# Performance work log

Measured on AMD Instinct MI355X. Metric: run time of the kernel, lower is better.

## Reference

```python
import jax, jax.numpy as jnp
import numpy as np

B, S, D = 2, 2048, 1024
H = 16
DK = D // H
LW = 256          # local window size
GSTRIDE = 64      # global downsample stride
SW = 512          # sliding window size
EPS = 1e-5
SCALE = 1.0 / np.sqrt(DK)


def _layernorm(x, g, b):
    mu = jnp.mean(x, axis=-1, keepdims=True)
    var = jnp.mean(jnp.square(x - mu), axis=-1, keepdims=True)
    return (x - mu) * jax.lax.rsqrt(var + EPS) * g + b


def setup_inputs() -> dict:
    key = jax.random.key(0)
    ks = jax.random.split(key, 16)
    std = 0.02
    def lin(k, din, dout):
        kw, kb = jax.random.split(k)
        return (jax.random.normal(kw, (din, dout), jnp.float32) * std,
                jax.random.normal(kb, (dout,), jnp.float32) * std)
    inp = {}
    inp["x"] = jax.random.normal(ks[0], (B, S, D), jnp.float32)
    # hierarchical attention params
    inp["lq_w"], inp["lq_b"] = lin(ks[1], D, D)
    inp["lk_w"], inp["lk_b"] = lin(ks[2], D, D)
    inp["lv_w"], inp["lv_b"] = lin(ks[3], D, D)
    inp["gq_w"], inp["gq_b"] = lin(ks[4], D, D)
    inp["gk_w"], inp["gk_b"] = lin(ks[5], D, D)
    inp["gv_w"], inp["gv_b"] = lin(ks[6], D, D)
    inp["h_out_w"], inp["h_out_b"] = lin(ks[7], 2 * D, D)
    inp["h_ln_g"] = jnp.ones((D,), jnp.float32)
    inp["h_ln_b"] = jnp.zeros((D,), jnp.float32)
    # sliding window attention params
    inp["sq_w"], inp["sq_b"] = lin(ks[8], D, D)
    inp["sk_w"], inp["sk_b"] = lin(ks[9], D, D)
    inp["sv_w"], inp["sv_b"] = lin(ks[10], D, D)
    inp["s_out_w"], inp["s_out_b"] = lin(ks[11], D, D)
    # combination
    inp["comb_w"], inp["comb_b"] = lin(ks[12], 2 * D, D)
    inp["ln_g"] = jnp.ones((D,), jnp.float32)
    inp["ln_b"] = jnp.zeros((D,), jnp.float32)
    return inp


def _forward(x, lq_w, lq_b, lk_w, lk_b, lv_w, lv_b,
             gq_w, gq_b, gk_w, gk_b, gv_w, gv_b,
             h_out_w, h_out_b, h_ln_g, h_ln_b,
             sq_w, sq_b, sk_w, sk_b, sv_w, sv_b,
             s_out_w, s_out_b, comb_w, comb_b, ln_g, ln_b):
    nw = S // LW  # seq_len is a multiple of LW (no padding needed)

    # ---- Hierarchical: local windowed attention (vectorized over windows) ----
    xw = x.reshape(B, nw, LW, D)
    lq = (xw @ lq_w + lq_b).reshape(B, nw, LW, H, DK)
    lk = (xw @ lk_w + lk_b).reshape(B, nw, LW, H, DK)
    lv = (xw @ lv_w + lv_b).reshape(B, nw, LW, H, DK)
    lsc = jnp.einsum('bnqhd,bnkhd->bnhqk', lq, lk) * SCALE
    lat = jax.nn.softmax(lsc, axis=-1)
    local_out = jnp.einsum('bnhqk,bnkhd->bnqhd', lat, lv).reshape(B, S, D)

    # ---- Hierarchical: global attention over strided downsample ----
    gc = x[:, ::GSTRIDE]                 # [B, G, D], G = S // GSTRIDE
    G = gc.shape[1]
    gq = (x @ gq_w + gq_b).reshape(B, S, H, DK)
    gk = (gc @ gk_w + gk_b).reshape(B, G, H, DK)
    gv = (gc @ gv_w + gv_b).reshape(B, G, H, DK)
    gsc = jnp.einsum('bqhd,bkhd->bhqk', gq, gk) * SCALE
    gat = jax.nn.softmax(gsc, axis=-1)
    global_out = jnp.einsum('bhqk,bkhd->bqhd', gat, gv).reshape(B, S, D)

    h_comb = jnp.concatenate([local_out, global_out], axis=-1) @ h_out_w + h_out_b
    h_out = _layernorm(x + h_comb, h_ln_g, h_ln_b)

    # ---- Sliding window attention ----
    sq = (x @ sq_w + sq_b).reshape(B, S, H, DK)
    sk = (x @ sk_w + sk_b).reshape(B, S, H, DK)
    sv = (x @ sv_w + sv_b).reshape(B, S, H, DK)
    ssc = jnp.einsum('bqhd,bkhd->bhqk', sq, sk) * SCALE
    idx = jnp.arange(S)
    half = SW // 2
    band = jnp.abs(idx[:, None] - idx[None, :]) <= half   # [S, S]
    ssc = jnp.where(band[None, None], ssc, -jnp.inf)
    sat = jax.nn.softmax(ssc, axis=-1)
    s_attn = jnp.einsum('bhqk,bkhd->bqhd', sat, sv).reshape(B, S, D)
    s_out = s_attn @ s_out_w + s_out_b

    # ---- combine scales ----
    combined = jnp.concatenate([h_out, s_out], axis=-1) @ comb_w + comb_b
    return _layernorm(x + combined, ln_g, ln_b)


def reference(x, lq_w, lq_b, lk_w, lk_b, lv_w, lv_b,
              gq_w, gq_b, gk_w, gk_b, gv_w, gv_b,
              h_out_w, h_out_b, h_ln_g, h_ln_b,
              sq_w, sq_b, sk_w, sk_b, sv_w, sv_b,
              s_out_w, s_out_b, comb_w, comb_b, ln_g, ln_b):
    return _forward(x, lq_w, lq_b, lk_w, lk_b, lv_w, lv_b,
                    gq_w, gq_b, gk_w, gk_b, gv_w, gv_b,
                    h_out_w, h_out_b, h_ln_g, h_ln_b,
                    sq_w, sq_b, sk_w, sk_b, sv_w, sv_b,
                    s_out_w, s_out_b, comb_w, comb_b, ln_g, ln_b)
```

## Files before the change

### kernel.cpp

```cpp
#include <hip/hip_runtime.h>

#define BATCH 2
#define SEQ   2048
#define DIM   1024
#define NH    16
#define DK    64
#define SCALE_F 0.125f
#define MASKED  -2e30f
#define MINIT   -1e30f

typedef __attribute__((ext_vector_type(4))) float f4;
typedef __attribute__((ext_vector_type(4))) float f32x4;
typedef __attribute__((ext_vector_type(8))) short s16x8;
typedef __attribute__((ext_vector_type(4))) int  i32x4;
typedef __attribute__((ext_vector_type(4))) unsigned short u16x4;

__device__ __forceinline__ float bf2f(unsigned short u){ return __uint_as_float(((unsigned)u) << 16); }
__device__ __forceinline__ unsigned short f2bf(float f){
  unsigned u = __float_as_uint(f);
  u += 0x7FFFu + ((u >> 16) & 1u);
  return (unsigned short)(u >> 16);
}

#define ASYNC_LDS16(g, l) \
  __builtin_amdgcn_global_load_lds((const __attribute__((address_space(1))) void*)(g), \
                                   (__attribute__((address_space(3))) void*)(l), 16, 0, 0)

__global__ __launch_bounds__(256) void cast_bf16_kernel(const float* __restrict__ in,
                                                        unsigned short* __restrict__ out, int n){
  int i = (blockIdx.x * 256 + threadIdx.x) * 4;
  if (i < n){
    f4 v = *(const f4*)&in[i];
    u16x4 o = { f2bf(v[0]), f2bf(v[1]), f2bf(v[2]), f2bf(v[3]) };
    *(u16x4*)&out[i] = o;
  }
}

struct TCP { const float* w[12]; unsigned short* wt[12]; };
__global__ __launch_bounds__(256) void transpose_cast_b(TCP P, int K){
  const float* W = P.w[blockIdx.z];
  unsigned short* Wt = P.wt[blockIdx.z];
  __shared__ float tile[32][33];
  int x = threadIdx.x & 31, y = threadIdx.x >> 5;
  int bc = blockIdx.x << 5;
  int br = blockIdx.y << 5;
  #pragma unroll
  for (int yy = y; yy < 32; yy += 8)
    tile[yy][x] = W[(size_t)(br + yy) * DIM + bc + x];
  __syncthreads();
  #pragma unroll
  for (int yy = y; yy < 32; yy += 8)
    Wt[(size_t)(bc + yy) * K + br + x] = f2bf(tile[x][yy]);
}

__global__ __launch_bounds__(256) void gc_extract(const float* __restrict__ x,
                                                  unsigned short* __restrict__ gcb){
  int row = blockIdx.x;
  int t = threadIdx.x;
  unsigned short* dst = gcb + (size_t)row * DIM;
  if (row < BATCH * 32){
    int b = row >> 5, g = row & 31;
    const float* src = x + ((size_t)b * SEQ + (size_t)g * 64) * DIM;
    f4 v = *(const f4*)&src[t * 4];
    u16x4 o = { f2bf(v[0]), f2bf(v[1]), f2bf(v[2]), f2bf(v[3]) };
    *(u16x4*)&dst[t * 4] = o;
  } else {
    u16x4 z = { 0, 0, 0, 0 };
    *(u16x4*)&dst[t * 4] = z;
  }
}

struct GOut { unsigned short* ob; float* of; const float* bias; int ld; int tr; };
struct GOuts { GOut d[4]; };

template<int BN>
__global__ __launch_bounds__(256) void gemm_bf16(
    const unsigned short* __restrict__ A, const unsigned short* __restrict__ Bt,
    GOuts descs, int K)
{
  constexpr int NF = BN / 32;
  __shared__ __align__(16) unsigned short As[2][128 * 32];
  __shared__ __align__(16) unsigned short Bs[2][BN * 32];
  const int tid = threadIdx.x;
  const int lane = tid & 63;
  const int w = tid >> 6;
  const int wr = w >> 1, wc = w & 1;
  const int gx = gridDim.x;
  const int nwg = gx * gridDim.y;
  const int orig = blockIdx.y * gx + blockIdx.x;
  const int swz = (orig & 7) * (nwg >> 3) + (orig >> 3);
  const int tx = swz % gx, ty = swz / gx;
  const int tm = ty << 7, tn = tx * BN;
  const GOut dsc = descs.d[tn >> 10];
  const int trans = dsc.tr;

  const int r0 = tid >> 2;
  const int ksw = (((tid & 3) ^ ((tid >> 3) & 3)) << 3);
  const unsigned short* Ag0 = A + (size_t)(tm + r0) * K + ksw;
  const unsigned short* Ag1 = A + (size_t)(tm + r0 + 64) * K + ksw;
  const unsigned short* Bg0 = Bt + (size_t)(tn + r0) * K + ksw;
  const unsigned short* Bg1 = Bt + (size_t)(tn + r0 + 64) * K + ksw;

  f32x4 acc[4][NF];
  #pragma unroll
  for (int m = 0; m < 4; ++m)
    #pragma unroll
    for (int n = 0; n < NF; ++n) acc[m][n] = (f32x4){0.f, 0.f, 0.f, 0.f};

  const int fr = lane & 15, fg = lane >> 4;
  const int kro = ((fg ^ ((fr >> 1) & 3)) << 3);

  auto STAGE = [&](int buf, int t){
    const int kk = t * 32;
    ASYNC_LDS16(Ag0 + kk, &As[buf][w * 512]);
    ASYNC_LDS16(Ag1 + kk, &As[buf][w * 512 + 2048]);
    ASYNC_LDS16(Bg0 + kk, &Bs[buf][w * 512]);
    if constexpr (BN == 128) ASYNC_LDS16(Bg1 + kk, &Bs[buf][w * 512 + 2048]);
  };
  auto COMPUTE = [&](int buf){
    s16x8 af[4], bfv[NF];
    #pragma unroll
    for (int m = 0; m < 4; ++m)
      af[m] = *(const s16x8*)&As[buf][(wr * 64 + m * 16 + fr) * 32 + kro];
    #pragma unroll
    for (int n = 0; n < NF; ++n)
      bfv[n] = *(const s16x8*)&Bs[buf][(wc * (BN / 2) + n * 16 + fr) * 32 + kro];
    if (trans){
      #pragma unroll
      for (int m = 0; m < 4; ++m)
        #pragma unroll
        for (int n = 0; n < NF; ++n)
          acc[m][n] = __builtin_amdgcn_mfma_f32_16x16x32_bf16(bfv[n], af[m], acc[m][n], 0, 0, 0);
    } else {
      #pragma unroll
      for (int m = 0; m < 4; ++m)
        #pragma unroll
        for (int n = 0; n < NF; ++n)
          acc[m][n] = __builtin_amdgcn_mfma_f32_16x16x32_bf16(af[m], bfv[n], acc[m][n], 0, 0, 0);
    }
  };

  const int nt = K >> 5;
  STAGE(0, 0);
  STAGE(1, 1);
  for (int t = 0; t < nt - 1; ++t){
    const int cur = t & 1;
    if constexpr (BN == 128) asm volatile("s_waitcnt vmcnt(4)" ::: "memory");
    else                     asm volatile("s_waitcnt vmcnt(3)" ::: "memory");
    __builtin_amdgcn_s_barrier();
    __builtin_amdgcn_sched_barrier(0);
    COMPUTE(cur);
    __builtin_amdgcn_sched_barrier(0);
    __builtin_amdgcn_s_barrier();
    __builtin_amdgcn_sched_barrier(0);
    if (t + 2 < nt) STAGE(cur, t + 2);
  }
  asm volatile("s_waitcnt vmcnt(0)" ::: "memory");
  __builtin_amdgcn_s_barrier();
  __builtin_amdgcn_sched_barrier(0);
  COMPUTE((nt - 1) & 1);

  #pragma unroll
  for (int m = 0; m < 4; ++m){
    #pragma unroll
    for (int n = 0; n < NF; ++n){
      if (!trans){
        int cl = (tn + wc * (BN / 2) + n * 16 + fr) & 1023;
        float bv = dsc.bias ? dsc.bias[cl] : 0.f;
        #pragma unroll
        for (int r = 0; r < 4; ++r){
          int row = tm + wr * 64 + m * 16 + fg * 4 + r;
          float v = acc[m][n][r] + bv;
          if (dsc.of) dsc.of[(size_t)row * dsc.ld + cl] = v;
          if (dsc.ob) dsc.ob[(size_t)row * dsc.ld + cl] = f2bf(v);
        }
      } else {
        int colT = tm + wr * 64 + m * 16 + fr;
        #pragma unroll
        for (int r = 0; r < 4; ++r){
          int dl = (tn + wc * (BN / 2) + n * 16 + fg * 4 + r) & 1023;
          float v = acc[m][n][r] + (dsc.bias ? dsc.bias[dl] : 0.f);
          dsc.ob[(size_t)dl * dsc.ld + colT] = f2bf(v);
        }
      }
    }
  }
}

template<int MODE>
__global__ __launch_bounds__(256) void mfma_attn(
    const unsigned short* __restrict__ Qb,
    const unsigned short* __restrict__ Kb,
    const unsigned short* __restrict__ Vtb, int ldvt,
    unsigned short* __restrict__ Out, int ldo, int ocol)
{
  __shared__ __align__(16) unsigned short Ks[64][72];
  __shared__ __align__(16) unsigned short Vs[64][72];
  __shared__ __align__(16) unsigned short Pl[4][16][72];
  const int tid = threadIdx.x, lane = tid & 63, wv = tid >> 6;
  const int fr = lane & 15, fg = lane >> 4;
  const int blk = blockIdx.x;
  const int h  = blk & 15;
  const int qc = (blk >> 4) & 31;
  const int b  = blk >> 9;
  const int q0 = qc * 64;
  const int tq0 = b * SEQ + q0;
  int jlo, ntile;
  if (MODE == 0){ jlo = (qc >> 2) << 8; ntile = 4; }
  else if (MODE == 1){
    jlo = q0 - 256 < 0 ? 0 : q0 - 256;
    int jhi = q0 + 320 > SEQ ? SEQ : q0 + 320;
    ntile = (jhi - jlo) >> 6;
  } else { jlo = 0; ntile = 1; }
  const int ktok0 = (MODE == 2) ? b * 32 : b * SEQ;

  s16x8 qf[2];
  {
    const size_t qrow = (size_t)(tq0 + wv * 16 + fr) * DIM + h * DK;
    qf[0] = *(const s16x8*)&Qb[qrow + fg * 8];
    qf[1] = *(const s16x8*)&Qb[qrow + 32 + fg * 8];
  }
  f32x4 of[4];
  #pragma unroll
  for (int dt = 0; dt < 4; ++dt) of[dt] = (f32x4){0.f, 0.f, 0.f, 0.f};
  f32x4 m4 = (f32x4){MINIT, MINIT, MINIT, MINIT};
  f32x4 l4 = (f32x4){0.f, 0.f, 0.f, 0.f};

  for (int t = 0; t < ntile; ++t){
    const int jb = jlo + t * 64;
    __syncthreads();
    #pragma unroll
    for (int p = 0; p < 2; ++p){
      int idx = p * 256 + tid;
      int row = idx >> 3, c8 = idx & 7;
      *(i32x4*)&Ks[row][c8 * 8] =
          *(const i32x4*)&Kb[(size_t)(ktok0 + jb + row) * DIM + h * DK + c8 * 8];
      i32x4 v = *(const i32x4*)&Vtb[(size_t)(h * DK + row) * ldvt + ktok0 + jb + c8 * 8];
      *(i32x4*)((char*)Vs + row * 144 + ((c8 * 16) ^ ((row & 7) << 4))) = v;
    }
    __syncthreads();
    f32x4 sf[4];
    #pragma unroll
    for (int t16 = 0; t16 < 4; ++t16){
      sf[t16] = (f32x4){0.f, 0.f, 0.f, 0.f};
      #pragma unroll
      for (int ks = 0; ks < 2; ++ks){
        s16x8 kf = *(const s16x8*)&Ks[t16 * 16 + fr][ks * 32 + fg * 8];
        sf[t16] = __builtin_amdgcn_mfma_f32_16x16x32_bf16(qf[ks], kf, sf[t16], 0, 0, 0);
      }
    }
    #pragma unroll
    for (int t16 = 0; t16 < 4; ++t16){
      int j = jb + t16 * 16 + fr;
      #pragma unroll
      for (int r = 0; r < 4; ++r){
        float v = sf[t16][r] * SCALE_F;
        bool valid = true;
        if (MODE == 1){ int dq = (q0 + wv * 16 + fg * 4 + r) - j; valid = (dq <= 256) && (dq >= -256); }
        if (MODE == 2){ valid = j < 32; }
        sf[t16][r] = valid ? v : MASKED;
      }
    }
    f32x4 mx;
    #pragma unroll
    for (int r = 0; r < 4; ++r)
      mx[r] = fmaxf(fmaxf(sf[0][r], sf[1][r]), fmaxf(sf[2][r], sf[3][r]));
    #pragma unroll
    for (int off = 1; off < 16; off <<= 1){
      #pragma unroll
      for (int r = 0; r < 4; ++r) mx[r] = fmaxf(mx[r], __shfl_xor(mx[r], off));
    }
    f32x4 sc;
    #pragma unroll
    for (int r = 0; r < 4; ++r){
      float mn = fmaxf(m4[r], mx[r]);
      sc[r] = __expf(m4[r] - mn);
      m4[r] = mn;
    }
    f32x4 sm = (f32x4){0.f, 0.f, 0.f, 0.f};
    #pragma unroll
    for (int t16 = 0; t16 < 4; ++t16){
      #pragma unroll
      for (int r = 0; r < 4; ++r){
        float e = __expf(sf[t16][r] - m4[r]);
        sm[r] += e;
        Pl[wv][fg * 4 + r][t16 * 16 + fr] = f2bf(e);
      }
    }
    #pragma unroll
    for (int off = 1; off < 16; off <<= 1){
      #pragma unroll
      for (int r = 0; r < 4; ++r) sm[r] += __shfl_xor(sm[r], off);
    }
    #pragma unroll
    for (int r = 0; r < 4; ++r) l4[r] = l4[r] * sc[r] + sm[r];
    #pragma unroll
    for (int dt = 0; dt < 4; ++dt)
      #pragma unroll
      for (int r = 0; r < 4; ++r) of[dt][r] *= sc[r];
    #pragma unroll
    for (int ks2 = 0; ks2 < 2; ++ks2){
      s16x8 pa = *(const s16x8*)&Pl[wv][fr][ks2 * 32 + fg * 8];
      #pragma unroll
      for (int dt = 0; dt < 4; ++dt){
        int d = dt * 16 + fr;
        s16x8 vf = *(const s16x8*)((char*)Vs + d * 144 + ((ks2 * 64 + fg * 16) ^ ((d & 7) << 4)));
        of[dt] = __builtin_amdgcn_mfma_f32_16x16x32_bf16(pa, vf, of[dt], 0, 0, 0);
      }
    }
  }
  #pragma unroll
  for (int dt = 0; dt < 4; ++dt){
    #pragma unroll
    for (int r = 0; r < 4; ++r){
      float val = of[dt][r] / l4[r];
      int q = tq0 + wv * 16 + fg * 4 + r;
      Out[(size_t)q * ldo + ocol + h * DK + dt * 16 + fr] = f2bf(val);
    }
  }
}

__global__ __launch_bounds__(256) void ln_fused(
    const float* __restrict__ x, const float* __restrict__ dlt,
    const float* __restrict__ g, const float* __restrict__ bta,
    float* __restrict__ outf, unsigned short* __restrict__ outb, int ldo)
{
  const int row = blockIdx.x;
  const int t = threadIdx.x, lane = t & 63, wv = t >> 6;
  const float* xr = x + (size_t)row * DIM;
  const float* dr = dlt + (size_t)row * DIM;
  f4 xv = *(const f4*)&xr[t * 4];
  f4 dv = *(const f4*)&dr[t * 4];
  f4 y = xv + dv;
  float s = y[0] + y[1] + y[2] + y[3];
  float ss = y[0]*y[0] + y[1]*y[1] + y[2]*y[2] + y[3]*y[3];
  #pragma unroll
  for (int off = 1; off < 64; off <<= 1){ s += __shfl_xor(s, off); ss += __shfl_xor(ss, off); }
  __shared__ float red[8];
  if (lane == 0){ red[wv] = s; red[wv + 4] = ss; }
  __syncthreads();
  float S = red[0] + red[1] + red[2] + red[3];
  float SS = red[4] + red[5] + red[6] + red[7];
  float mu = S * (1.f / DIM);
  float var = SS * (1.f / DIM) - mu * mu;
  float rs = rsqrtf(var + 1e-5f);
  f4 gv = *(const f4*)&g[t * 4];
  f4 bv = *(const f4*)&bta[t * 4];
  f4 o;
  #pragma unroll
  for (int i = 0; i < 4; ++i) o[i] = (y[i] - mu) * rs * gv[i] + bv[i];
  if (outf) *(f4*)&outf[(size_t)row * ldo + t * 4] = o;
  if (outb){
    u16x4 ob = { f2bf(o[0]), f2bf(o[1]), f2bf(o[2]), f2bf(o[3]) };
    *(u16x4*)&outb[(size_t)row * ldo + t * 4] = ob;
  }
}

extern "C" void kernel_launch(void* const* d_in, const int* in_sizes, int n_in,
                              void* d_out, int out_size, void* d_ws, size_t ws_size,
                              hipStream_t stream){
  (void)in_sizes; (void)n_in; (void)out_size; (void)ws_size;
  const float* x      = (const float*)d_in[0];
  const float* lq_w   = (const float*)d_in[1];  const float* lq_b  = (const float*)d_in[2];
  const float* lk_w   = (const float*)d_in[3];  const float* lk_b  = (const float*)d_in[4];
  const float* lv_w   = (const float*)d_in[5];  const float* lv_b  = (const float*)d_in[6];
  const float* gq_w   = (const float*)d_in[7];  const float* gq_b  = (const float*)d_in[8];
  const float* gk_w   = (const float*)d_in[9];  const float* gk_b  = (const float*)d_in[10];
  const float* gv_w   = (const float*)d_in[11]; const float* gv_b  = (const float*)d_in[12];
  const float* ho_w   = (const float*)d_in[13]; const float* ho_b  = (const float*)d_in[14];
  const float* hln_g  = (const float*)d_in[15]; const float* hln_b = (const float*)d_in[16];
  const float* sq_w   = (const float*)d_in[17]; const float* sq_b  = (const float*)d_in[18];
  const float* sk_w   = (const float*)d_in[19]; const float* sk_b  = (const float*)d_in[20];
  const float* sv_w   = (const float*)d_in[21]; const float* sv_b  = (const float*)d_in[22];
  const float* so_w   = (const float*)d_in[23]; const float* so_b  = (const float*)d_in[24];
  const float* cb_w   = (const float*)d_in[25]; const float* cb_b  = (const float*)d_in[26];
  const float* ln_g   = (const float*)d_in[27]; const float* ln_b  = (const float*)d_in[28];

  const size_t M = (size_t)BATCH * SEQ;
  const size_t W1 = (size_t)DIM * DIM;
  char* ws = (char*)d_ws;
  size_t off = 0;
  auto alloc = [&](size_t bytes) -> void* {
    void* p = ws + off; off += (bytes + 255) & ~(size_t)255; return p;
  };
  unsigned short* xb    = (unsigned short*)alloc(M * DIM * 2);
  unsigned short* wt_s  = (unsigned short*)alloc(3 * W1 * 2);
  unsigned short* wt_lg = (unsigned short*)alloc(4 * W1 * 2);
  unsigned short* wt_g2 = (unsigned short*)alloc(2 * W1 * 2);
  unsigned short* wt_so = (unsigned short*)alloc(W1 * 2);
  unsigned short* wt_ho = (unsigned short*)alloc(2 * W1 * 2);
  unsigned short* wt_cb = (unsigned short*)alloc(2 * W1 * 2);
  unsigned short* gcb   = (unsigned short*)alloc((size_t)128 * DIM * 2);
  unsigned short* qb    = (unsigned short*)alloc(M * DIM * 2);
  unsigned short* kb    = (unsigned short*)alloc(M * DIM * 2);
  unsigned short* vtb   = (unsigned short*)alloc(M * DIM * 2);
  unsigned short* qg    = (unsigned short*)alloc(M * DIM * 2);
  unsigned short* gkb   = (unsigned short*)alloc((size_t)128 * DIM * 2);
  unsigned short* vtg   = (unsigned short*)alloc((size_t)128 * DIM * 2);
  unsigned short* satt  = (unsigned short*)alloc(M * DIM * 2);
  unsigned short* hcat  = (unsigned short*)alloc(M * 2 * DIM * 2);
  unsigned short* ccat  = (unsigned short*)alloc(M * 2 * DIM * 2);
  float* Af             = (float*)alloc(M * DIM * 4);

  dim3 b256(256);
  cast_bf16_kernel<<<dim3((M * DIM) / 1024), b256, 0, stream>>>(x, xb, (int)(M * DIM));
  {
    TCP p1 = {};
    const float* ws_[10] = {sq_w, sk_w, sv_w, lq_w, lk_w, lv_w, gq_w, gk_w, gv_w, so_w};
    unsigned short* wts_[10] = {wt_s, wt_s + W1, wt_s + 2 * W1,
                                wt_lg, wt_lg + W1, wt_lg + 2 * W1, wt_lg + 3 * W1,
                                wt_g2, wt_g2 + W1, wt_so};
    for (int i = 0; i < 10; ++i){ p1.w[i] = ws_[i]; p1.wt[i] = wts_[i]; }
    transpose_cast_b<<<dim3(32, 32, 10), b256, 0, stream>>>(p1, DIM);
    TCP p2 = {};
    p2.w[0] = ho_w; p2.wt[0] = wt_ho;
    p2.w[1] = cb_w; p2.wt[1] = wt_cb;
    transpose_cast_b<<<dim3(32, 64, 2), b256, 0, stream>>>(p2, 2 * DIM);
  }
  gc_extract<<<dim3(128), b256, 0, stream>>>(x, gcb);

  dim3 attn_grid(1024);
  auto mk = [&](unsigned short* ob, float* of, const float* bias, int ld, int tr) -> GOut {
    GOut g; g.ob = ob; g.of = of; g.bias = bias; g.ld = ld; g.tr = tr; return g;
  };

  {
    GOuts ds = {};
    ds.d[0] = mk(qb,  nullptr, sq_b, DIM, 0);
    ds.d[1] = mk(kb,  nullptr, sk_b, DIM, 0);
    ds.d[2] = mk(vtb, nullptr, sv_b, (int)M, 1);
    gemm_bf16<128><<<dim3(24, 32), b256, 0, stream>>>(xb, wt_s, ds, DIM);
  }
  mfma_attn<1><<<attn_grid, b256, 0, stream>>>(qb, kb, vtb, (int)M, satt, DIM, 0);

  {
    GOuts ds = {};
    ds.d[0] = mk(qb,  nullptr, lq_b, DIM, 0);
    ds.d[1] = mk(kb,  nullptr, lk_b, DIM, 0);
    ds.d[2] = mk(vtb, nullptr, lv_b, (int)M, 1);
    ds.d[3] = mk(qg,  nullptr, gq_b, DIM, 0);
    gemm_bf16<128><<<dim3(32, 32), b256, 0, stream>>>(xb, wt_lg, ds, DIM);
  }
  {
    GOuts ds = {};
    ds.d[0] = mk(ccat + 1024, nullptr, so_b, 2 * DIM, 0);
    gemm_bf16<64><<<dim3(16, 32), b256, 0, stream>>>(satt, wt_so, ds, DIM);
  }
  mfma_attn<0><<<attn_grid, b256, 0, stream>>>(qb, kb, vtb, (int)M, hcat, 2 * DIM, 0);

  {
    GOuts ds = {};
    ds.d[0] = mk(gkb, nullptr, gk_b, DIM, 0);
    ds.d[1] = mk(vtg, nullptr, gv_b, 128, 1);
    gemm_bf16<128><<<dim3(16, 1), b256, 0, stream>>>(gcb, wt_g2, ds, DIM);
  }
  mfma_attn<2><<<attn_grid, b256, 0, stream>>>(qg, gkb, vtg, 128, hcat, 2 * DIM, 1024);

  {
    GOuts ds = {};
    ds.d[0] = mk(nullptr, Af, ho_b, DIM, 0);
    gemm_bf16<64><<<dim3(16, 32), b256, 0, stream>>>(hcat, wt_ho, ds, 2 * DIM);
  }
  ln_fused<<<dim3((int)M), b256, 0, stream>>>(x, Af, hln_g, hln_b, nullptr, ccat, 2 * DIM);

  {
    GOuts ds = {};
    ds.d[0] = mk(nullptr, Af, cb_b, DIM, 0);
    gemm_bf16<64><<<dim3(16, 32), b256, 0, stream>>>(ccat, wt_cb, ds, 2 * DIM);
  }
  ln_fused<<<dim3((int)M), b256, 0, stream>>>(x, Af, ln_g, ln_b, (float*)d_out, nullptr, DIM);
}
```

Baseline: 525.2 us.

## Add 256x256-tile 512-thread GEMM kernel for fused QKV projections

Adds a new bf16 MFMA GEMM kernel with 256x256 output tiles, 8 waves, double-buffered async LDS staging with an XOR swizzle, and a grouped tile-order remap. It replaces the 128-tile GEMM for the sliding-window QKV projection and the local/global QKV projection. The larger tiles raise arithmetic intensity and cut global reloads of A and B. The cost is fewer workgroups (192 and 256 blocks), which may underfill the CUs, and 128 KB of LDS per block, which is likely to limit occupancy below the requested two blocks per CU.

```diff
diff --git a/kernel.cpp b/kernel.cpp
--- a/kernel.cpp
+++ b/kernel.cpp
@@ -179,6 +179,125 @@
         #pragma unroll
         for (int r = 0; r < 4; ++r){
           int dl = (tn + wc * (BN / 2) + n * 16 + fg * 4 + r) & 1023;
+          float v = acc[m][n][r] + (dsc.bias ? dsc.bias[dl] : 0.f);
+          dsc.ob[(size_t)dl * dsc.ld + colT] = f2bf(v);
+        }
+      }
+    }
+  }
+}
+
+__global__ __launch_bounds__(512, 2) void gemm256(
+    const unsigned short* __restrict__ A, const unsigned short* __restrict__ Bt,
+    GOuts descs, int K)
+{
+  __shared__ __align__(16) unsigned short As[2][256 * 64];
+  __shared__ __align__(16) unsigned short Bs[2][256 * 64];
+  const int tid = threadIdx.x;
+  const int lane = tid & 63;
+  const int w = tid >> 6;
+  const int wr = w >> 2, wc = w & 3;
+  const int gx = gridDim.x;
+  const int nwg = gx * gridDim.y;
+  const int orig = blockIdx.y * gx + blockIdx.x;
+  const int swz = (orig & 7) * (nwg >> 3) + (orig >> 3);
+  const int tx = swz % gx, ty = swz / gx;
+  const int tm = ty << 8, tn = tx << 8;
+  const GOut dsc = descs.d[tn >> 10];
+  const int trans = dsc.tr;
+
+  const int sr = lane >> 3;
+  const int klog = (((lane & 7) ^ sr) << 3);
+  const unsigned short* Agp[4];
+  const unsigned short* Bgp[4];
+  #pragma unroll
+  for (int i = 0; i < 4; ++i){
+    const int s = w * 4 + i;
+    Agp[i] = A + (size_t)(tm + s * 8 + sr) * K + klog;
+    Bgp[i] = Bt + (size_t)(tn + s * 8 + sr) * K + klog;
+  }
+
+  f32x4 acc[8][4];
+  #pragma unroll
+  for (int m = 0; m < 8; ++m)
+    #pragma unroll
+    for (int n = 0; n < 4; ++n) acc[m][n] = (f32x4){0.f, 0.f, 0.f, 0.f};
+
+  const int fr = lane & 15, fg = lane >> 4;
+
+  auto STAGE = [&](int buf, int t){
+    const int kk = t * 64;
+    #pragma unroll
+    for (int i = 0; i < 4; ++i){
+      ASYNC_LDS16(Agp[i] + kk, &As[buf][(w * 4 + i) * 512]);
+      ASYNC_LDS16(Bgp[i] + kk, &Bs[buf][(w * 4 + i) * 512]);
+    }
+  };
+  auto COMPUTE = [&](int buf){
+    #pragma unroll
+    for (int ks = 0; ks < 2; ++ks){
+      const int rc = (((ks * 4 + fg) ^ (fr & 7)) << 3);
+      s16x8 af[8], bfv[4];
+      #pragma unroll
+      for (int m = 0; m < 8; ++m)
+        af[m] = *(const s16x8*)&As[buf][(wr * 128 + m * 16 + fr) * 64 + rc];
+      #pragma unroll
+      for (int n = 0; n < 4; ++n)
+        bfv[n] = *(const s16x8*)&Bs[buf][(wc * 64 + n * 16 + fr) * 64 + rc];
+      if (trans){
+        #pragma unroll
+        for (int m = 0; m < 8; ++m)
+          #pragma unroll
+          for (int n = 0; n < 4; ++n)
+            acc[m][n] = __builtin_amdgcn_mfma_f32_16x16x32_bf16(bfv[n], af[m], acc[m][n], 0, 0, 0);
+      } else {
+        #pragma unroll
+        for (int m = 0; m < 8; ++m)
+          #pragma unroll
+          for (int n = 0; n < 4; ++n)
+            acc[m][n] = __builtin_amdgcn_mfma_f32_16x16x32_bf16(af[m], bfv[n], acc[m][n], 0, 0, 0);
+      }
+    }
+  };
+
+  const int nt = K >> 6;
+  STAGE(0, 0);
+  STAGE(1, 1);
+  for (int t = 0; t < nt - 1; ++t){
+    const int cur = t & 1;
+    asm volatile("s_waitcnt vmcnt(8)" ::: "memory");
+    __builtin_amdgcn_s_barrier();
+    __builtin_amdgcn_sched_barrier(0);
+    COMPUTE(cur);
+    __builtin_amdgcn_sched_barrier(0);
+    __builtin_amdgcn_s_barrier();
+    __builtin_amdgcn_sched_barrier(0);
+    if (t + 2 < nt) STAGE(cur, t + 2);
+  }
+  asm volatile("s_waitcnt vmcnt(0)" ::: "memory");
+  __builtin_amdgcn_s_barrier();
+  __builtin_amdgcn_sched_barrier(0);
+  COMPUTE((nt - 1) & 1);
+
+  #pragma unroll
+  for (int m = 0; m < 8; ++m){
+    #pragma unroll
+    for (int n = 0; n < 4; ++n){
+      if (!trans){
+        int cl = (tn + wc * 64 + n * 16 + fr) & 1023;
+        float bv = dsc.bias ? dsc.bias[cl] : 0.f;
+        #pragma unroll
+        for (int r = 0; r < 4; ++r){
+          int row = tm + wr * 128 + m * 16 + fg * 4 + r;
+          float v = acc[m][n][r] + bv;
+          if (dsc.of) dsc.of[(size_t)row * dsc.ld + cl] = v;
+          if (dsc.ob) dsc.ob[(size_t)row * dsc.ld + cl] = f2bf(v);
+        }
+      } else {
+        int colT = tm + wr * 128 + m * 16 + fr;
+        #pragma unroll
+        for (int r = 0; r < 4; ++r){
+          int dl = (tn + wc * 64 + n * 16 + fg * 4 + r) & 1023;
           float v = acc[m][n][r] + (dsc.bias ? dsc.bias[dl] : 0.f);
           dsc.ob[(size_t)dl * dsc.ld + colT] = f2bf(v);
         }
@@ -403,6 +522,7 @@
   float* Af             = (float*)alloc(M * DIM * 4);
 
   dim3 b256(256);
+  dim3 b512(512);
   cast_bf16_kernel<<<dim3((M * DIM) / 1024), b256, 0, stream>>>(x, xb, (int)(M * DIM));
   {
     TCP p1 = {};
@@ -429,7 +549,7 @@
     ds.d[0] = mk(qb,  nullptr, sq_b, DIM, 0);
     ds.d[1] = mk(kb,  nullptr, sk_b, DIM, 0);
     ds.d[2] = mk(vtb, nullptr, sv_b, (int)M, 1);
-    gemm_bf16<128><<<dim3(24, 32), b256, 0, stream>>>(xb, wt_s, ds, DIM);
+    gemm256<<<dim3(12, 16), b512, 0, stream>>>(xb, wt_s, ds, DIM);
   }
   mfma_attn<1><<<attn_grid, b256, 0, stream>>>(qb, kb, vtb, (int)M, satt, DIM, 0);
 
@@ -439,7 +559,7 @@
     ds.d[1] = mk(kb,  nullptr, lk_b, DIM, 0);
     ds.d[2] = mk(vtb, nullptr, lv_b, (int)M, 1);
     ds.d[3] = mk(qg,  nullptr, gq_b, DIM, 0);
-    gemm_bf16<128><<<dim3(32, 32), b256, 0, stream>>>(xb, wt_lg, ds, DIM);
+    gemm256<<<dim3(16, 16), b512, 0, stream>>>(xb, wt_lg, ds, DIM);
   }
   {
     GOuts ds = {};
```

After: 912.9 us. 1.74x slower.
